# Performance work log

Measured on AMD Instinct MI355X. Metric: run time of the kernel, lower is better.

The kernel has to match this reference:

```python
import jax, jax.numpy as jnp
import numpy as np

N_AA = 300000
N_PROT = 30000
D_AA = 128
D_PROT = 128
HID = 128
OUT = 64
E_AP = 300000
E_PP = 960000
BATCH = 16384
NEG_SLOPE = 0.2


def _gatv2(x_src, x_dst, src, dst, Wl, bl, Wr, br, att, bias, num_dst):
    # GATv2Conv (heads=1): e_ij = att . leaky_relu(Wl x_j + Wr x_i); softmax over dst; out_i = sum alpha_ij * (Wl x_j) + bias
    xl = x_src @ Wl + bl                      # [Ns, C]
    xr = x_dst @ Wr + br                      # [Nd, C]
    e = jax.nn.leaky_relu(xl[src] + xr[dst], NEG_SLOPE)   # [E, C]
    logits = e @ att                          # [E]
    lmax = jax.ops.segment_max(logits, dst, num_segments=num_dst)
    ex = jnp.exp(logits - lmax[dst])
    denom = jax.ops.segment_sum(ex, dst, num_segments=num_dst)
    alpha = ex / denom[dst]                   # [E]
    msg = xl[src] * alpha[:, None]            # [E, C]
    out = jax.ops.segment_sum(msg, dst, num_segments=num_dst)
    return out + bias


def setup_inputs() -> dict:
    key = jax.random.key(0)
    ks = jax.random.split(key, 16)
    s = 0.05
    x_aa = jax.random.normal(ks[0], (N_AA, D_AA), jnp.float32)
    x_prot = jax.random.normal(ks[1], (N_PROT, D_PROT), jnp.float32)
    edge_index_ap = jnp.stack([
        jax.random.randint(ks[2], (E_AP,), 0, N_AA),
        jax.random.randint(ks[3], (E_AP,), 0, N_PROT)])
    edge_index_pp = jnp.stack([
        jax.random.randint(ks[4], (E_PP,), 0, N_PROT),
        jax.random.randint(ks[5], (E_PP,), 0, N_PROT)])
    return {
        'x_aa': x_aa, 'x_prot': x_prot,
        'edge_index_ap': edge_index_ap, 'edge_index_pp': edge_index_pp,
        'batch_size': BATCH,
        'Wl_ap': s * jax.random.normal(ks[6], (D_AA, HID), jnp.float32),
        'bl_ap': jnp.zeros((HID,), jnp.float32),
        'Wr_ap': s * jax.random.normal(ks[7], (D_PROT, HID), jnp.float32),
        'br_ap': jnp.zeros((HID,), jnp.float32),
        'att_ap': s * jax.random.normal(ks[8], (HID,), jnp.float32),
        'bias_ap': jnp.zeros((HID,), jnp.float32),
        'Wl_pp': s * jax.random.normal(ks[9], (D_PROT, HID), jnp.float32),
        'bl_pp': jnp.zeros((HID,), jnp.float32),
        'Wr_pp': s * jax.random.normal(ks[10], (D_PROT, HID), jnp.float32),
        'br_pp': jnp.zeros((HID,), jnp.float32),
        'att_pp': s * jax.random.normal(ks[11], (HID,), jnp.float32),
        'bias_pp': jnp.zeros((HID,), jnp.float32),
        'W_lin': s * jax.random.normal(ks[12], (HID, OUT), jnp.float32),
        'b_lin': jnp.zeros((OUT,), jnp.float32),
    }


def reference(x_aa, x_prot, edge_index_ap, edge_index_pp, batch_size,
              Wl_ap, bl_ap, Wr_ap, br_ap, att_ap, bias_ap,
              Wl_pp, bl_pp, Wr_pp, br_pp, att_pp, bias_pp,
              W_lin, b_lin):
    out_ap = _gatv2(x_aa, x_prot, edge_index_ap[0], edge_index_ap[1],
                    Wl_ap, bl_ap, Wr_ap, br_ap, att_ap, bias_ap, N_PROT)
    out_pp = _gatv2(x_prot, x_prot, edge_index_pp[0], edge_index_pp[1],
                    Wl_pp, bl_pp, Wr_pp, br_pp, att_pp, bias_pp, N_PROT)
    x = out_ap + out_pp                      # HeteroConv aggr='sum'
    x = jax.nn.relu(x[:batch_size])
    return x @ W_lin + b_lin
```

## Files before the change

kernel.cpp:

```cpp
#include <hip/hip_runtime.h>
#include <hip/hip_bf16.h>

typedef __attribute__((ext_vector_type(8))) short short8;
typedef __attribute__((ext_vector_type(4))) unsigned short ushort4_t;
typedef __attribute__((ext_vector_type(4))) float f32x4;

#define CAP_AP 64
#define CAP_PP 128

__device__ __forceinline__ unsigned short f2bf(float f) {
  unsigned u = __float_as_uint(f);
  u += 0x7FFFu + ((u >> 16) & 1u);
  return (unsigned short)(u >> 16);
}

__global__ __launch_bounds__(256) void k_init(
    int* __restrict__ map, int* __restrict__ cnt_ap, int* __restrict__ cnt_pp,
    int* __restrict__ ccount, int n_aa, int batch)
{
  int i = blockIdx.x * 256 + threadIdx.x;
  if (i < n_aa) map[i] = -1;
  if (i < batch) { cnt_ap[i] = 0; cnt_pp[i] = 0; }
  if (i == 0) *ccount = 0;
}

__global__ __launch_bounds__(256) void k_edges(
    const int* __restrict__ ei_ap, const int* __restrict__ ei_pp,
    int* __restrict__ map, int* __restrict__ cnt_ap, int* __restrict__ cnt_pp,
    int* __restrict__ csr_ap, int* __restrict__ csr_pp,
    int e_ap, int e_pp, int nb_ap, int batch)
{
  int b = blockIdx.x;
  if (b < nb_ap) {
    int e = b * 256 + threadIdx.x;
    if (e < e_ap) {
      int d = ei_ap[e_ap + e];
      if (d < batch) {
        int s = ei_ap[e];
        int pos = atomicAdd(&cnt_ap[d], 1);
        if (pos < CAP_AP) csr_ap[d * CAP_AP + pos] = s;
        map[s] = 1;
      }
    }
  } else {
    int e = (b - nb_ap) * 256 + threadIdx.x;
    if (e < e_pp) {
      int d = ei_pp[e_pp + e];
      if (d < batch) {
        int pos = atomicAdd(&cnt_pp[d], 1);
        if (pos < CAP_PP) csr_pp[d * CAP_PP + pos] = ei_pp[e];
      }
    }
  }
}

__global__ __launch_bounds__(256) void k_assign(
    int* __restrict__ map, int* __restrict__ inv, int* __restrict__ ccount, int n)
{
  int i = blockIdx.x * 256 + threadIdx.x;
  bool need = (i < n) && (map[i] == 1);
  unsigned long long m = __ballot(need);
  if (m == 0ull) return;
  int lane = threadIdx.x & 63;
  int pre = __popcll(m & ((1ull << lane) - 1ull));
  int leader = __ffsll((unsigned long long)m) - 1;
  int base = 0;
  if (lane == leader) base = atomicAdd(ccount, __popcll(m));
  base = __shfl(base, leader, 64);
  if (need) {
    int slot = base + pre;
    map[i] = slot;
    inv[slot] = i;
  }
}

struct GemmJob {
  const float* X; const int* inv; const int* rowsp; int M;
  const float* W; const float* bias; unsigned short* Y; int nb;
};

__device__ __forceinline__ void gemm_body(const GemmJob& J, int bid, short8* lwb)
{
  const int tid = threadIdx.x;
  const int rows = J.rowsp ? *J.rowsp : J.M;

  {
    unsigned short* lw16 = (unsigned short*)lwb;
#pragma unroll
    for (int p = 0; p < 16; ++p) {
      int fi = p * 1024 + tid * 4;
      float4 w4 = *(const float4*)(J.W + fi);
#pragma unroll
      for (int q = 0; q < 4; ++q) {
        int k = (fi + q) >> 7, n = (fi + q) & 127;
        float wv = (q == 0) ? w4.x : (q == 1) ? w4.y : (q == 2) ? w4.z : w4.w;
        lw16[(((k >> 5) * 8 + (n >> 4)) * 64 + ((k >> 3) & 3) * 16 + (n & 15)) * 8 + (k & 7)] = f2bf(wv);
      }
    }
  }

  const int wave = tid >> 6;
  const int lane = tid & 63;
  const int quad = lane >> 4;
  const int l16  = lane & 15;
  __syncthreads();

  for (int tile = bid; tile * 64 < rows; tile += J.nb) {
    int ra = tile * 64 + wave * 16 + l16;
    long xrow = -1;
    if (ra < rows) xrow = J.inv ? (long)J.inv[ra] : (long)ra;

    short8 xf[4];
#pragma unroll
    for (int kt = 0; kt < 4; ++kt) {
      short8 a = {};
      if (xrow >= 0) {
        const float* p = J.X + xrow * 128 + kt * 32 + quad * 8;
        float4 x0 = ((const float4*)p)[0];
        float4 x1 = ((const float4*)p)[1];
        a[0] = (short)f2bf(x0.x); a[1] = (short)f2bf(x0.y);
        a[2] = (short)f2bf(x0.z); a[3] = (short)f2bf(x0.w);
        a[4] = (short)f2bf(x1.x); a[5] = (short)f2bf(x1.y);
        a[6] = (short)f2bf(x1.z); a[7] = (short)f2bf(x1.w);
      }
      xf[kt] = a;
    }

    f32x4 accs[8];
#pragma unroll
    for (int nt = 0; nt < 8; ++nt) {
      f32x4 acc = {0.f, 0.f, 0.f, 0.f};
#pragma unroll
      for (int kt = 0; kt < 4; ++kt)
        acc = __builtin_amdgcn_mfma_f32_16x16x32_bf16(lwb[(kt * 8 + nt) * 64 + lane], xf[kt], acc, 0, 0, 0);
      accs[nt] = acc;
    }

    if (ra < rows) {
      unsigned short* yp = J.Y + (long)ra * 128;
#pragma unroll
      for (int nt = 0; nt < 8; ++nt) {
        int col = nt * 16 + quad * 4;
        float4 bv = *(const float4*)(J.bias + col);
        ushort4_t v;
        v[0] = f2bf(accs[nt][0] + bv.x);
        v[1] = f2bf(accs[nt][1] + bv.y);
        v[2] = f2bf(accs[nt][2] + bv.z);
        v[3] = f2bf(accs[nt][3] + bv.w);
        *(ushort4_t*)(yp + col) = v;
      }
    }
  }
}

__global__ __launch_bounds__(256) void k_mega(
    GemmJob j0, GemmJob j1, GemmJob j2, GemmJob j3,
    const int* __restrict__ map, const int* __restrict__ cnt_ap,
    int* __restrict__ csr_ap, int nb_gemm, int nb_remap, int batch)
{
  __shared__ short8 lwb[4 * 8 * 64];
  int b = blockIdx.x;
  if (b < nb_gemm) {
    if (b < j0.nb)                      gemm_body(j0, b, lwb);
    else if (b < j0.nb + j1.nb)         gemm_body(j1, b - j0.nb, lwb);
    else if (b < j0.nb + j1.nb + j2.nb) gemm_body(j2, b - j0.nb - j1.nb, lwb);
    else                                gemm_body(j3, b - j0.nb - j1.nb - j2.nb, lwb);
  } else {
    int i = (b - nb_gemm) * 256 + threadIdx.x;
    if (i < batch * CAP_AP) {
      int d = i / CAP_AP;
      int slot = i - d * CAP_AP;
      int n = cnt_ap[d]; if (n > CAP_AP) n = CAP_AP;
      if (slot < n) csr_ap[i] = map[csr_ap[i]];
    }
  }
}

__global__ __launch_bounds__(256) void k_gat_final(
    const int* __restrict__ cnt_ap, const int* __restrict__ csr_ap,
    const unsigned short* __restrict__ xl_aa,
    const unsigned short* __restrict__ xr_ap, const float* __restrict__ att_ap,
    const int* __restrict__ cnt_pp, const int* __restrict__ csr_pp,
    const unsigned short* __restrict__ xl_pp,
    const unsigned short* __restrict__ xr_pp, const float* __restrict__ att_pp,
    const float* __restrict__ bias_ap, const float* __restrict__ bias_pp,
    const float* __restrict__ W_lin, const float* __restrict__ b_lin,
    float* __restrict__ out, int batch)
{
  __shared__ unsigned lw2[64 * 64];
  __shared__ float lh[4][128];
  for (int e = threadIdx.x; e < 4096; e += 256) {
    int cp = e >> 6, o = e & 63;
    unsigned lo = f2bf(W_lin[(2 * cp) * 64 + o]);
    unsigned hi = f2bf(W_lin[(2 * cp + 1) * 64 + o]);
    lw2[e] = lo | (hi << 16);
  }

  const int wave = threadIdx.x >> 6;
  const int lane = threadIdx.x & 63;
  const int dst = blockIdx.x * 4 + wave;
  const int c0 = 2 * lane;

  float h0 = 0.f, h1 = 0.f;
  if (dst < batch) {
    h0 = bias_ap[c0] + bias_pp[c0];
    h1 = bias_ap[c0 + 1] + bias_pp[c0 + 1];

#pragma unroll
    for (int type = 0; type < 2; ++type) {
      const int* cnt  = type ? cnt_pp : cnt_ap;
      const int* csr  = type ? csr_pp : csr_ap;
      const int cap   = type ? CAP_PP : CAP_AP;
      const unsigned short* xl = type ? xl_pp : xl_aa;
      const unsigned short* xr = type ? xr_pp : xr_ap;
      const float* att = type ? att_pp : att_ap;

      int n = __builtin_amdgcn_readfirstlane(cnt[dst]);
      if (n > cap) n = cap;
      const long base = (long)dst * cap;
      unsigned upr = *(const unsigned*)(xr + (long)dst * 128 + c0);
      float xr0 = __uint_as_float(upr << 16);
      float xr1 = __uint_as_float(upr & 0xffff0000u);
      float2 at = *(const float2*)(att + c0);

      float l = 0.f, o0 = 0.f, o1 = 0.f;
      int j = 0;
      for (; j + 4 <= n; j += 4) {
        int si[4]; unsigned u[4];
#pragma unroll
        for (int q = 0; q < 4; ++q) si[q] = csr[base + j + q];
#pragma unroll
        for (int q = 0; q < 4; ++q)
          u[q] = *(const unsigned*)(xl + (long)si[q] * 128 + c0);
        float pv[4], a0v[4], a1v[4];
#pragma unroll
        for (int q = 0; q < 4; ++q) {
          float a0 = __uint_as_float(u[q] << 16);
          float a1 = __uint_as_float(u[q] & 0xffff0000u);
          a0v[q] = a0; a1v[q] = a1;
          float e0 = a0 + xr0; e0 = e0 > 0.f ? e0 : 0.2f * e0;
          float e1 = a1 + xr1; e1 = e1 > 0.f ? e1 : 0.2f * e1;
          pv[q] = at.x * e0 + at.y * e1;
        }
#pragma unroll
        for (int off = 32; off; off >>= 1) {
#pragma unroll
          for (int q = 0; q < 4; ++q) pv[q] += __shfl_xor(pv[q], off, 64);
        }
#pragma unroll
        for (int q = 0; q < 4; ++q) {
          float w = __expf(pv[q]);
          l += w;
          o0 = fmaf(w, a0v[q], o0);
          o1 = fmaf(w, a1v[q], o1);
        }
      }
      for (; j < n; ++j) {
        int sA = csr[base + j];
        unsigned uA = *(const unsigned*)(xl + (long)sA * 128 + c0);
        float a0 = __uint_as_float(uA << 16), a1 = __uint_as_float(uA & 0xffff0000u);
        float e0 = a0 + xr0; e0 = e0 > 0.f ? e0 : 0.2f * e0;
        float e1 = a1 + xr1; e1 = e1 > 0.f ? e1 : 0.2f * e1;
        float pA = at.x * e0 + at.y * e1;
#pragma unroll
        for (int off = 32; off; off >>= 1) pA += __shfl_xor(pA, off, 64);
        float w = __expf(pA);
        l += w;
        o0 = fmaf(w, a0, o0);
        o1 = fmaf(w, a1, o1);
      }
      float invl = (l > 0.f) ? 1.f / l : 0.f;
      h0 = fmaf(o0, invl, h0);
      h1 = fmaf(o1, invl, h1);
    }
  }

  lh[wave][c0]     = h0 > 0.f ? h0 : 0.f;
  lh[wave][c0 + 1] = h1 > 0.f ? h1 : 0.f;
  __syncthreads();

  if (dst < batch) {
    float acc = b_lin[lane];
#pragma unroll 16
    for (int cp = 0; cp < 64; ++cp) {
      unsigned u = lw2[cp * 64 + lane];
      acc = fmaf(lh[wave][2 * cp],     __uint_as_float(u << 16),        acc);
      acc = fmaf(lh[wave][2 * cp + 1], __uint_as_float(u & 0xffff0000u), acc);
    }
    out[(long)dst * 64 + lane] = acc;
  }
}

extern "C" void kernel_launch(void* const* d_in, const int* in_sizes, int n_in,
                              void* d_out, int out_size, void* d_ws, size_t ws_size,
                              hipStream_t stream)
{
  const float* x_aa   = (const float*)d_in[0];
  const float* x_prot = (const float*)d_in[1];
  const int*   ei_ap  = (const int*)d_in[2];
  const int*   ei_pp  = (const int*)d_in[3];
  const float* Wl_ap  = (const float*)d_in[5];
  const float* bl_ap  = (const float*)d_in[6];
  const float* Wr_ap  = (const float*)d_in[7];
  const float* br_ap  = (const float*)d_in[8];
  const float* att_ap = (const float*)d_in[9];
  const float* bias_ap= (const float*)d_in[10];
  const float* Wl_pp  = (const float*)d_in[11];
  const float* bl_pp  = (const float*)d_in[12];
  const float* Wr_pp  = (const float*)d_in[13];
  const float* br_pp  = (const float*)d_in[14];
  const float* att_pp = (const float*)d_in[15];
  const float* bias_pp= (const float*)d_in[16];
  const float* W_lin  = (const float*)d_in[17];
  const float* b_lin  = (const float*)d_in[18];
  float* out = (float*)d_out;

  const int D = 128;
  const int n_aa   = in_sizes[0] / D;
  const int n_prot = in_sizes[1] / D;
  const int e_ap   = in_sizes[2] / 2;
  const int e_pp   = in_sizes[3] / 2;
  const int batch  = out_size / 64;

  char* p = (char*)d_ws;
  auto take = [&](size_t n) { char* r = p; p += (n + 255) & ~(size_t)255; return r; };
  unsigned short* xlc_aa = (unsigned short*)take((size_t)n_aa * D * 2);
  unsigned short* xl_pp  = (unsigned short*)take((size_t)n_prot * D * 2);
  unsigned short* xr_ap  = (unsigned short*)take((size_t)batch * D * 2);
  unsigned short* xr_pp  = (unsigned short*)take((size_t)batch * D * 2);
  int* map      = (int*)take((size_t)n_aa * 4);
  int* inv      = (int*)take((size_t)n_aa * 4);
  int* ccount   = (int*)take(4);
  int* cnt_ap   = (int*)take((size_t)batch * 4);
  int* cnt_pp   = (int*)take((size_t)batch * 4);
  int* csr_ap   = (int*)take((size_t)batch * CAP_AP * 4);
  int* csr_pp   = (int*)take((size_t)batch * CAP_PP * 4);
  (void)ws_size; (void)n_in;

  const int nb_ap = (e_ap + 255) / 256;
  const int nb_pp = (e_pp + 255) / 256;
  const int nb_init = (n_aa + 255) / 256;

  k_init<<<nb_init, 256, 0, stream>>>(map, cnt_ap, cnt_pp, ccount, n_aa, batch);
  k_edges<<<nb_ap + nb_pp, 256, 0, stream>>>(
      ei_ap, ei_pp, map, cnt_ap, cnt_pp, csr_ap, csr_pp,
      e_ap, e_pp, nb_ap, batch);
  k_assign<<<nb_init, 256, 0, stream>>>(map, inv, ccount, n_aa);

  GemmJob j0{x_aa,   inv,     ccount,  0,      Wl_ap, bl_ap, xlc_aa, 1024};
  GemmJob j1{x_prot, nullptr, nullptr, n_prot, Wl_pp, bl_pp, xl_pp,  (n_prot + 63) / 64};
  GemmJob j2{x_prot, nullptr, nullptr, batch,  Wr_ap, br_ap, xr_ap,  (batch + 63) / 64};
  GemmJob j3{x_prot, nullptr, nullptr, batch,  Wr_pp, br_pp, xr_pp,  (batch + 63) / 64};
  const int nb_gemm = j0.nb + j1.nb + j2.nb + j3.nb;
  const int nb_remap = (batch * CAP_AP + 255) / 256;
  k_mega<<<nb_gemm + nb_remap, 256, 0, stream>>>(
      j0, j1, j2, j3, map, cnt_ap, csr_ap, nb_gemm, nb_remap, batch);

  k_gat_final<<<(batch + 3) / 4, 256, 0, stream>>>(
      cnt_ap, csr_ap, xlc_aa, xr_ap, att_ap,
      cnt_pp, csr_pp, xl_pp, xr_pp, att_pp,
      bias_ap, bias_pp, W_lin, b_lin, out, batch);
}
```

Measured before the change: 475.9 us.

## Shard edge buckets, assign compact ids inline, and drop init/assign/remap kernels

Edge buckets are split into four shards per destination so fewer atomics contend on one counter, and each shard is capped at 32 entries. Compact source ids are now assigned inside the edge kernel with atomicCAS, and the gather looks ids up through the map, which removes the init, assign and remap passes. Init work moves to memsets, the weight staging writes packed bf16 pairs, and the GEMM grid sizes are retuned. In exchange, global atomics on a single counter add contention, slot order becomes nondeterministic, and the gather pays an extra indirection per aa edge.

After: 543.1 us. 1.14x slower.

```diff
diff --git a/kernel.cpp b/kernel.cpp
--- a/kernel.cpp
+++ b/kernel.cpp
@@ -5,8 +5,8 @@
 typedef __attribute__((ext_vector_type(4))) unsigned short ushort4_t;
 typedef __attribute__((ext_vector_type(4))) float f32x4;
 
-#define CAP_AP 64
-#define CAP_PP 128
+#define NSH 4
+#define SCAP 32
 
 __device__ __forceinline__ unsigned short f2bf(float f) {
   unsigned u = __float_as_uint(f);
@@ -14,19 +14,10 @@
   return (unsigned short)(u >> 16);
 }
 
-__global__ __launch_bounds__(256) void k_init(
-    int* __restrict__ map, int* __restrict__ cnt_ap, int* __restrict__ cnt_pp,
-    int* __restrict__ ccount, int n_aa, int batch)
-{
-  int i = blockIdx.x * 256 + threadIdx.x;
-  if (i < n_aa) map[i] = -1;
-  if (i < batch) { cnt_ap[i] = 0; cnt_pp[i] = 0; }
-  if (i == 0) *ccount = 0;
-}
-
 __global__ __launch_bounds__(256) void k_edges(
     const int* __restrict__ ei_ap, const int* __restrict__ ei_pp,
-    int* __restrict__ map, int* __restrict__ cnt_ap, int* __restrict__ cnt_pp,
+    int* __restrict__ map, int* __restrict__ inv, int* __restrict__ ccount,
+    int* __restrict__ cnt_ap, int* __restrict__ cnt_pp,
     int* __restrict__ csr_ap, int* __restrict__ csr_pp,
     int e_ap, int e_pp, int nb_ap, int batch)
 {
@@ -37,9 +28,14 @@
       int d = ei_ap[e_ap + e];
       if (d < batch) {
         int s = ei_ap[e];
-        int pos = atomicAdd(&cnt_ap[d], 1);
-        if (pos < CAP_AP) csr_ap[d * CAP_AP + pos] = s;
-        map[s] = 1;
+        int sh = e & (NSH - 1);
+        int pos = atomicAdd(&cnt_ap[d * NSH + sh], 1);
+        if (pos < SCAP) csr_ap[(d * NSH + sh) * SCAP + pos] = s;
+        if (atomicCAS(&map[s], -1, -2) == -1) {
+          int slot = atomicAdd(ccount, 1);
+          map[s] = slot;
+          inv[slot] = s;
+        }
       }
     }
   } else {
@@ -47,30 +43,11 @@
     if (e < e_pp) {
       int d = ei_pp[e_pp + e];
       if (d < batch) {
-        int pos = atomicAdd(&cnt_pp[d], 1);
-        if (pos < CAP_PP) csr_pp[d * CAP_PP + pos] = ei_pp[e];
-      }
-    }
-  }
-}
-
-__global__ __launch_bounds__(256) void k_assign(
-    int* __restrict__ map, int* __restrict__ inv, int* __restrict__ ccount, int n)
-{
-  int i = blockIdx.x * 256 + threadIdx.x;
-  bool need = (i < n) && (map[i] == 1);
-  unsigned long long m = __ballot(need);
-  if (m == 0ull) return;
-  int lane = threadIdx.x & 63;
-  int pre = __popcll(m & ((1ull << lane) - 1ull));
-  int leader = __ffsll((unsigned long long)m) - 1;
-  int base = 0;
-  if (lane == leader) base = atomicAdd(ccount, __popcll(m));
-  base = __shfl(base, leader, 64);
-  if (need) {
-    int slot = base + pre;
-    map[i] = slot;
-    inv[slot] = i;
+        int sh = e & (NSH - 1);
+        int pos = atomicAdd(&cnt_pp[d * NSH + sh], 1);
+        if (pos < SCAP) csr_pp[(d * NSH + sh) * SCAP + pos] = ei_pp[e];
+      }
+    }
   }
 }
 
@@ -85,16 +62,25 @@
   const int rows = J.rowsp ? *J.rowsp : J.M;
 
   {
-    unsigned short* lw16 = (unsigned short*)lwb;
-#pragma unroll
-    for (int p = 0; p < 16; ++p) {
-      int fi = p * 1024 + tid * 4;
-      float4 w4 = *(const float4*)(J.W + fi);
+    unsigned* lw32 = (unsigned*)lwb;
+#pragma unroll
+    for (int p = 0; p < 8; ++p) {
+      int slot = p * 256 + tid;
+      int kp   = slot >> 5;
+      int n4   = (slot & 31) * 4;
+      int k = 2 * kp;
+      float4 wa = *(const float4*)(J.W + k * 128 + n4);
+      float4 wb = *(const float4*)(J.W + (k + 1) * 128 + n4);
+      int frag = (k >> 5) * 8 + (n4 >> 4);
+      int lbase = ((k >> 3) & 3) * 16;
+      int j = k & 7;
+      const float* fa = (const float*)&wa;
+      const float* fb = (const float*)&wb;
 #pragma unroll
       for (int q = 0; q < 4; ++q) {
-        int k = (fi + q) >> 7, n = (fi + q) & 127;
-        float wv = (q == 0) ? w4.x : (q == 1) ? w4.y : (q == 2) ? w4.z : w4.w;
-        lw16[(((k >> 5) * 8 + (n >> 4)) * 64 + ((k >> 3) & 3) * 16 + (n & 15)) * 8 + (k & 7)] = f2bf(wv);
+        int lane_ = lbase + ((n4 + q) & 15);
+        unsigned pk = (unsigned)f2bf(fa[q]) | ((unsigned)f2bf(fb[q]) << 16);
+        lw32[(frag * 64 + lane_) * 4 + (j >> 1)] = pk;
       }
     }
   }
@@ -153,32 +139,93 @@
   }
 }
 
-__global__ __launch_bounds__(256) void k_mega(
-    GemmJob j0, GemmJob j1, GemmJob j2, GemmJob j3,
-    const int* __restrict__ map, const int* __restrict__ cnt_ap,
-    int* __restrict__ csr_ap, int nb_gemm, int nb_remap, int batch)
+__global__ __launch_bounds__(256) void k_gemms(
+    GemmJob j0, GemmJob j1, GemmJob j2, GemmJob j3)
 {
   __shared__ short8 lwb[4 * 8 * 64];
   int b = blockIdx.x;
-  if (b < nb_gemm) {
-    if (b < j0.nb)                      gemm_body(j0, b, lwb);
-    else if (b < j0.nb + j1.nb)         gemm_body(j1, b - j0.nb, lwb);
-    else if (b < j0.nb + j1.nb + j2.nb) gemm_body(j2, b - j0.nb - j1.nb, lwb);
-    else                                gemm_body(j3, b - j0.nb - j1.nb - j2.nb, lwb);
-  } else {
-    int i = (b - nb_gemm) * 256 + threadIdx.x;
-    if (i < batch * CAP_AP) {
-      int d = i / CAP_AP;
-      int slot = i - d * CAP_AP;
-      int n = cnt_ap[d]; if (n > CAP_AP) n = CAP_AP;
-      if (slot < n) csr_ap[i] = map[csr_ap[i]];
-    }
-  }
+  if (b < j0.nb)                      gemm_body(j0, b, lwb);
+  else if (b < j0.nb + j1.nb)         gemm_body(j1, b - j0.nb, lwb);
+  else if (b < j0.nb + j1.nb + j2.nb) gemm_body(j2, b - j0.nb - j1.nb, lwb);
+  else                                gemm_body(j3, b - j0.nb - j1.nb - j2.nb, lwb);
+}
+
+__device__ __forceinline__ void gat_type(
+    int dst, int c0, const int* __restrict__ cnt, const int* __restrict__ csr,
+    const int* __restrict__ map, const unsigned short* __restrict__ xl,
+    const unsigned short* __restrict__ xr, const float* __restrict__ att,
+    float& h0, float& h1)
+{
+  int n[NSH];
+  {
+    int4 c4 = *(const int4*)(cnt + dst * NSH);
+    int v0 = c4.x < SCAP ? c4.x : SCAP;
+    int v1 = c4.y < SCAP ? c4.y : SCAP;
+    int v2 = c4.z < SCAP ? c4.z : SCAP;
+    int v3 = c4.w < SCAP ? c4.w : SCAP;
+    n[0] = __builtin_amdgcn_readfirstlane(v0);
+    n[1] = __builtin_amdgcn_readfirstlane(v1);
+    n[2] = __builtin_amdgcn_readfirstlane(v2);
+    n[3] = __builtin_amdgcn_readfirstlane(v3);
+  }
+  int nmax = n[0];
+#pragma unroll
+  for (int s = 1; s < NSH; ++s) nmax = n[s] > nmax ? n[s] : nmax;
+
+  unsigned upr = *(const unsigned*)(xr + (long)dst * 128 + c0);
+  float xr0 = __uint_as_float(upr << 16);
+  float xr1 = __uint_as_float(upr & 0xffff0000u);
+  float2 at = *(const float2*)(att + c0);
+
+  const int base = dst * (NSH * SCAP);
+  float l = 0.f, o0 = 0.f, o1 = 0.f;
+
+  for (int t = 0; t < nmax; ++t) {
+    unsigned u[NSH];
+#pragma unroll
+    for (int s = 0; s < NSH; ++s) {
+      if (t < n[s]) {
+        int src = csr[base + s * SCAP + t];
+        if (map) src = map[src];
+        u[s] = *(const unsigned*)(xl + (long)src * 128 + c0);
+      }
+    }
+    float p[NSH], a0[NSH], a1[NSH];
+#pragma unroll
+    for (int s = 0; s < NSH; ++s) {
+      if (t < n[s]) {
+        float v0 = __uint_as_float(u[s] << 16);
+        float v1 = __uint_as_float(u[s] & 0xffff0000u);
+        a0[s] = v0; a1[s] = v1;
+        float e0 = v0 + xr0; e0 = e0 > 0.f ? e0 : 0.2f * e0;
+        float e1 = v1 + xr1; e1 = e1 > 0.f ? e1 : 0.2f * e1;
+        p[s] = at.x * e0 + at.y * e1;
+      }
+    }
+#pragma unroll
+    for (int off = 32; off; off >>= 1) {
+#pragma unroll
+      for (int s = 0; s < NSH; ++s)
+        if (t < n[s]) p[s] += __shfl_xor(p[s], off, 64);
+    }
+#pragma unroll
+    for (int s = 0; s < NSH; ++s) {
+      if (t < n[s]) {
+        float w = __expf(p[s]);
+        l += w;
+        o0 = fmaf(w, a0[s], o0);
+        o1 = fmaf(w, a1[s], o1);
+      }
+    }
+  }
+  float invl = (l > 0.f) ? 1.f / l : 0.f;
+  h0 = fmaf(o0, invl, h0);
+  h1 = fmaf(o1, invl, h1);
 }
 
 __global__ __launch_bounds__(256) void k_gat_final(
     const int* __restrict__ cnt_ap, const int* __restrict__ csr_ap,
-    const unsigned short* __restrict__ xl_aa,
+    const int* __restrict__ map, const unsigned short* __restrict__ xl_aa,
     const unsigned short* __restrict__ xr_ap, const float* __restrict__ att_ap,
     const int* __restrict__ cnt_pp, const int* __restrict__ csr_pp,
     const unsigned short* __restrict__ xl_pp,
@@ -205,74 +252,8 @@
   if (dst < batch) {
     h0 = bias_ap[c0] + bias_pp[c0];
     h1 = bias_ap[c0 + 1] + bias_pp[c0 + 1];
-
-#pragma unroll
-    for (int type = 0; type < 2; ++type) {
-      const int* cnt  = type ? cnt_pp : cnt_ap;
-      const int* csr  = type ? csr_pp : csr_ap;
-      const int cap   = type ? CAP_PP : CAP_AP;
-      const unsigned short* xl = type ? xl_pp : xl_aa;
-      const unsigned short* xr = type ? xr_pp : xr_ap;
-      const float* att = type ? att_pp : att_ap;
-
-      int n = __builtin_amdgcn_readfirstlane(cnt[dst]);
-      if (n > cap) n = cap;
-      const long base = (long)dst * cap;
-      unsigned upr = *(const unsigned*)(xr + (long)dst * 128 + c0);
-      float xr0 = __uint_as_float(upr << 16);
-      float xr1 = __uint_as_float(upr & 0xffff0000u);
-      float2 at = *(const float2*)(att + c0);
-
-      float l = 0.f, o0 = 0.f, o1 = 0.f;
-      int j = 0;
-      for (; j + 4 <= n; j += 4) {
-        int si[4]; unsigned u[4];
-#pragma unroll
-        for (int q = 0; q < 4; ++q) si[q] = csr[base + j + q];
-#pragma unroll
-        for (int q = 0; q < 4; ++q)
-          u[q] = *(const unsigned*)(xl + (long)si[q] * 128 + c0);
-        float pv[4], a0v[4], a1v[4];
-#pragma unroll
-        for (int q = 0; q < 4; ++q) {
-          float a0 = __uint_as_float(u[q] << 16);
-          float a1 = __uint_as_float(u[q] & 0xffff0000u);
-          a0v[q] = a0; a1v[q] = a1;
-          float e0 = a0 + xr0; e0 = e0 > 0.f ? e0 : 0.2f * e0;
-          float e1 = a1 + xr1; e1 = e1 > 0.f ? e1 : 0.2f * e1;
-          pv[q] = at.x * e0 + at.y * e1;
-        }
-#pragma unroll
-        for (int off = 32; off; off >>= 1) {
-#pragma unroll
-          for (int q = 0; q < 4; ++q) pv[q] += __shfl_xor(pv[q], off, 64);
-        }
-#pragma unroll
-        for (int q = 0; q < 4; ++q) {
-          float w = __expf(pv[q]);
-          l += w;
-          o0 = fmaf(w, a0v[q], o0);
-          o1 = fmaf(w, a1v[q], o1);
-        }
-      }
-      for (; j < n; ++j) {
-        int sA = csr[base + j];
-        unsigned uA = *(const unsigned*)(xl + (long)sA * 128 + c0);
-        float a0 = __uint_as_float(uA << 16), a1 = __uint_as_float(uA & 0xffff0000u);
-        float e0 = a0 + xr0; e0 = e0 > 0.f ? e0 : 0.2f * e0;
-        float e1 = a1 + xr1; e1 = e1 > 0.f ? e1 : 0.2f * e1;
-        float pA = at.x * e0 + at.y * e1;
-#pragma unroll
-        for (int off = 32; off; off >>= 1) pA += __shfl_xor(pA, off, 64);
-        float w = __expf(pA);
-        l += w;
-        o0 = fmaf(w, a0, o0);
-        o1 = fmaf(w, a1, o1);
-      }
-      float invl = (l > 0.f) ? 1.f / l : 0.f;
-      h0 = fmaf(o0, invl, h0);
-      h1 = fmaf(o1, invl, h1);
-    }
+    gat_type(dst, c0, cnt_ap, csr_ap, map,     xl_aa, xr_ap, att_ap, h0, h1);
+    gat_type(dst, c0, cnt_pp, csr_pp, nullptr, xl_pp, xr_pp, att_pp, h0, h1);
   }
 
   lh[wave][c0]     = h0 > 0.f ? h0 : 0.f;
@@ -284,7 +265,7 @@
 #pragma unroll 16
     for (int cp = 0; cp < 64; ++cp) {
       unsigned u = lw2[cp * 64 + lane];
-      acc = fmaf(lh[wave][2 * cp],     __uint_as_float(u << 16),        acc);
+      acc = fmaf(lh[wave][2 * cp],     __uint_as_float(u << 16),         acc);
       acc = fmaf(lh[wave][2 * cp + 1], __uint_as_float(u & 0xffff0000u), acc);
     }
     out[(long)dst * 64 + lane] = acc;
@@ -328,36 +309,34 @@
   unsigned short* xl_pp  = (unsigned short*)take((size_t)n_prot * D * 2);
   unsigned short* xr_ap  = (unsigned short*)take((size_t)batch * D * 2);
   unsigned short* xr_pp  = (unsigned short*)take((size_t)batch * D * 2);
-  int* map      = (int*)take((size_t)n_aa * 4);
-  int* inv      = (int*)take((size_t)n_aa * 4);
-  int* ccount   = (int*)take(4);
-  int* cnt_ap   = (int*)take((size_t)batch * 4);
-  int* cnt_pp   = (int*)take((size_t)batch * 4);
-  int* csr_ap   = (int*)take((size_t)batch * CAP_AP * 4);
-  int* csr_pp   = (int*)take((size_t)batch * CAP_PP * 4);
+  char* zreg   = take((size_t)batch * NSH * 4 * 2 + 256);
+  int* cnt_ap  = (int*)zreg;
+  int* cnt_pp  = cnt_ap + (size_t)batch * NSH;
+  int* ccount  = cnt_pp + (size_t)batch * NSH;
+  int* map     = (int*)take((size_t)n_aa * 4);
+  int* inv     = (int*)take((size_t)n_aa * 4);
+  int* csr_ap  = (int*)take((size_t)batch * NSH * SCAP * 4);
+  int* csr_pp  = (int*)take((size_t)batch * NSH * SCAP * 4);
   (void)ws_size; (void)n_in;
+
+  hipMemsetAsync(zreg, 0, (size_t)batch * NSH * 4 * 2 + 4, stream);
+  hipMemsetAsync(map, 0xFF, (size_t)n_aa * 4, stream);
 
   const int nb_ap = (e_ap + 255) / 256;
   const int nb_pp = (e_pp + 255) / 256;
-  const int nb_init = (n_aa + 255) / 256;
-
-  k_init<<<nb_init, 256, 0, stream>>>(map, cnt_ap, cnt_pp, ccount, n_aa, batch);
+
   k_edges<<<nb_ap + nb_pp, 256, 0, stream>>>(
-      ei_ap, ei_pp, map, cnt_ap, cnt_pp, csr_ap, csr_pp,
+      ei_ap, ei_pp, map, inv, ccount, cnt_ap, cnt_pp, csr_ap, csr_pp,
       e_ap, e_pp, nb_ap, batch);
-  k_assign<<<nb_init, 256, 0, stream>>>(map, inv, ccount, n_aa);
-
-  GemmJob j0{x_aa,   inv,     ccount,  0,      Wl_ap, bl_ap, xlc_aa, 1024};
-  GemmJob j1{x_prot, nullptr, nullptr, n_prot, Wl_pp, bl_pp, xl_pp,  (n_prot + 63) / 64};
-  GemmJob j2{x_prot, nullptr, nullptr, batch,  Wr_ap, br_ap, xr_ap,  (batch + 63) / 64};
-  GemmJob j3{x_prot, nullptr, nullptr, batch,  Wr_pp, br_pp, xr_pp,  (batch + 63) / 64};
-  const int nb_gemm = j0.nb + j1.nb + j2.nb + j3.nb;
-  const int nb_remap = (batch * CAP_AP + 255) / 256;
-  k_mega<<<nb_gemm + nb_remap, 256, 0, stream>>>(
-      j0, j1, j2, j3, map, cnt_ap, csr_ap, nb_gemm, nb_remap, batch);
+
+  GemmJob j0{x_aa,   inv,     ccount,  0,      Wl_ap, bl_ap, xlc_aa, 512};
+  GemmJob j1{x_prot, nullptr, nullptr, n_prot, Wl_pp, bl_pp, xl_pp,  224};
+  GemmJob j2{x_prot, nullptr, nullptr, batch,  Wr_ap, br_ap, xr_ap,  144};
+  GemmJob j3{x_prot, nullptr, nullptr, batch,  Wr_pp, br_pp, xr_pp,  144};
+  k_gemms<<<j0.nb + j1.nb + j2.nb + j3.nb, 256, 0, stream>>>(j0, j1, j2, j3);
 
   k_gat_final<<<(batch + 3) / 4, 256, 0, stream>>>(
-      cnt_ap, csr_ap, xlc_aa, xr_ap, att_ap,
+      cnt_ap, csr_ap, map, xlc_aa, xr_ap, att_ap,
       cnt_pp, csr_pp, xl_pp, xr_pp, att_pp,
       bias_ap, bias_pp, W_lin, b_lin, out, batch);
 }
```
